# Optimization experiments

Hardware: AMD Instinct MI355X
Metric: run time of the kernel (lower is better)

The kernel has to match this reference:

```python
import jax, jax.numpy as jnp
import numpy as np
from jax import lax

RANK = 8
ALPHA = 16.0
SCALING = ALPHA / RANK  # 2.0
C_IN, C_OUT, KH, KW = 128, 256, 3, 3


def setup_inputs() -> dict:
    key = jax.random.key(0)
    k1, k2, k3, k4, k5 = jax.random.split(key, 5)
    x = jax.random.normal(k1, (16, C_IN, 64, 64), dtype=jnp.float32)
    W = jax.random.normal(k2, (C_OUT, C_IN, KH, KW), dtype=jnp.float32) * 0.05
    b = jax.random.normal(k3, (C_OUT,), dtype=jnp.float32) * 0.05
    lora_A = jax.random.normal(k4, (RANK, C_IN * KH * KW), dtype=jnp.float32) * 0.02
    lora_B = jax.random.normal(k5, (C_OUT, RANK), dtype=jnp.float32) * 0.02
    return {"x": x, "W": W, "b": b, "lora_A": lora_A, "lora_B": lora_B}


def _conv(x, w, stride=(1, 1), padding=((1, 1), (1, 1))):
    return lax.conv_general_dilated(
        x, w, window_strides=stride, padding=padding,
        dimension_numbers=("NCHW", "OIHW", "NCHW"))


def reference(x, W, b, lora_A, lora_B):
    # Base (frozen) conv: [B, C_out, H, W]
    base_out = _conv(x, W) + b[None, :, None, None]
    # LoRA path. The torch code does im2col -> (BL, C_in*kh*kw) @ A.T @ B.T.
    # Because unfold flattens patches channel-major as (C_in, kh, kw), the
    # identical math is: rank-r conv with A reshaped as [rank, C_in, kh, kw],
    # then a 1x1 mix with B. Same result, no im2col materialization.
    A_k = lora_A.reshape(RANK, C_IN, KH, KW)
    h = _conv(x, A_k)                                   # [B, rank, H, W]
    lora_out = jnp.einsum("brhw,or->bohw", h, lora_B) * SCALING
    return base_out + lora_out
```

## Files before the change

kernel.cpp:

```cpp
#include <hip/hip_runtime.h>
#include <hip/hip_bf16.h>


#define CIN   128
#define COUT  256
#define NBAT  16
#define HPAD  66
#define WPAD  66

typedef __bf16 bf16x8 __attribute__((ext_vector_type(8)));
typedef float f32x4 __attribute__((ext_vector_type(4)));

#define XPAD_ELEMS ((size_t)NBAT * HPAD * WPAD * CIN)
#define XPAD_BYTES (XPAD_ELEMS * 2)
#define WT_ELEMS   ((size_t)9 * COUT * CIN)
#define WS_NEED    (XPAD_BYTES + WT_ELEMS * 2)

typedef __attribute__((address_space(1))) void gvoid;
typedef __attribute__((address_space(3))) void lvoid;

__device__ __forceinline__ void load_lds16(const void* g, void* l) {
    __builtin_amdgcn_global_load_lds((gvoid*)g, (lvoid*)l, 16, 0, 0);
}

__global__ void prep_w(const float* __restrict__ W, const float* __restrict__ lA,
                       const float* __restrict__ lB, __hip_bfloat16* __restrict__ Wt) {
    int idx = blockIdx.x * 256 + threadIdx.x;
    int c   = idx & 127;
    int o   = (idx >> 7) & 255;
    int tap = idx >> 15;
    float acc = W[(o * 128 + c) * 9 + tap];
    float s = 0.f;
#pragma unroll
    for (int r = 0; r < 8; ++r)
        s += lB[o * 8 + r] * lA[r * 1152 + c * 9 + tap];
    acc += 2.0f * s;
    Wt[idx] = __float2bfloat16(acc);
}

__global__ void pad_x(const float* __restrict__ x, __bf16* __restrict__ xpad) {
    __shared__ float tile[128][66];
    const int n = blockIdx.x >> 6;
    const int h = blockIdx.x & 63;
    const int t = threadIdx.x;
    const float* src = x + (size_t)n * 128 * 4096 + (size_t)h * 64;
#pragma unroll
    for (int i = 0; i < 8; ++i) {
        int g  = i * 256 + t;
        int c  = g >> 4;
        int w4 = (g & 15) * 4;
        const float4 v = *reinterpret_cast<const float4*>(src + (size_t)c * 4096 + w4);
        tile[c][w4 + 0] = v.x; tile[c][w4 + 1] = v.y;
        tile[c][w4 + 2] = v.z; tile[c][w4 + 3] = v.w;
    }
    __syncthreads();
    __bf16* dst = xpad + ((size_t)(n * 66 + h + 1) * 66 + 1) * 128;
#pragma unroll
    for (int i = 0; i < 4; ++i) {
        int g  = i * 256 + t;
        int w  = g >> 4;
        int c0 = (g & 15) * 8;
        bf16x8 v;
#pragma unroll
        for (int j = 0; j < 8; ++j) v[j] = (__bf16)tile[c0 + j][w];
        *reinterpret_cast<bf16x8*>(dst + (size_t)w * 128 + c0) = v;
    }
    bf16x8 z = {};
    __bf16* rowbase = xpad + (size_t)(n * 66 + h + 1) * 66 * 128;
    if (t < 32) {
        int ww = (t < 16) ? 0 : 65;
        int c0 = (t & 15) * 8;
        *reinterpret_cast<bf16x8*>(rowbase + (size_t)ww * 128 + c0) = z;
    }
    if (h == 0 || h == 63) {
        __bf16* hrow = xpad + (size_t)(n * 66 + (h == 0 ? 0 : 65)) * 66 * 128;
        for (int i = t; i < 66 * 16; i += 256)
            *reinterpret_cast<bf16x8*>(hrow + (size_t)i * 8) = z;
    }
}

__global__ void __launch_bounds__(256) conv_mfma(
    const __bf16* __restrict__ xpad, const __bf16* __restrict__ Wt,
    const float* __restrict__ bias, float* __restrict__ out) {
    __shared__ __align__(16) __bf16 As[128 * 64];
    __shared__ __align__(16) __bf16 Bs[128 * 64];

    const int tid  = threadIdx.x;
    const int wv   = tid >> 6;
    const int lane = tid & 63;

    const int pt    = blockIdx.x;
    const int ob    = blockIdx.y;
    const int n     = pt >> 5;
    const int h0    = (pt & 31) << 1;
    const int obase = ob << 7;

    const int swz = ((lane >> 3) << 7) + ((((lane & 7) ^ (lane >> 3)) & 7) << 3);

    const __bf16* aG[4];
    const __bf16* bG[4];
#pragma unroll
    for (int j = 0; j < 4; ++j) {
        const int row0 = wv * 32 + j * 8;
        aG[j] = Wt + (obase + row0) * 128 + swz;
        const int p0 = row0;
        bG[j] = xpad + (((size_t)(n * 66 + h0 + (p0 >> 6)) * 66 + (p0 & 63)) * 128) + swz;
    }

    const int wo = (wv >> 1) << 6;
    const int wp = (wv & 1) << 6;

    int arow[4], brow[4], qo[2];
#pragma unroll
    for (int i = 0; i < 4; ++i) {
        arow[i] = (wo + i * 16 + (lane & 15)) << 6;
        brow[i] = (wp + i * 16 + (lane & 15)) << 6;
    }
#pragma unroll
    for (int s = 0; s < 2; ++s)
        qo[s] = ((((lane >> 4) + s * 4) ^ (lane & 7)) << 3);

    f32x4 acc[4][4] = {};

#pragma unroll
    for (int tap = 0; tap < 9; ++tap) {
        const int kh = tap / 3, kw = tap % 3;
        const int aoff_t = tap * (COUT * CIN);
        const int boff_t = (kh * 66 + kw) * 128;
#pragma unroll
        for (int cb = 0; cb < 2; ++cb) {
            const int ao = aoff_t + cb * 64;
            const int bo = boff_t + cb * 64;
            __syncthreads();
#pragma unroll
            for (int j = 0; j < 4; ++j) {
                load_lds16(aG[j] + ao, &As[wv * 2048 + j * 512]);
                load_lds16(bG[j] + bo, &Bs[wv * 2048 + j * 512]);
            }
            __syncthreads();
#pragma unroll
            for (int s = 0; s < 2; ++s) {
                bf16x8 af[4], bfr[4];
#pragma unroll
                for (int i = 0; i < 4; ++i) {
                    af[i]  = *reinterpret_cast<const bf16x8*>(&As[arow[i] + qo[s]]);
                    bfr[i] = *reinterpret_cast<const bf16x8*>(&Bs[brow[i] + qo[s]]);
                }
#pragma unroll
                for (int mi = 0; mi < 4; ++mi)
#pragma unroll
                    for (int ni = 0; ni < 4; ++ni)
                        acc[mi][ni] = __builtin_amdgcn_mfma_f32_16x16x32_bf16(
                            af[mi], bfr[ni], acc[mi][ni], 0, 0, 0);
            }
        }
    }

    const int col  = lane & 15;
    const int orow = (lane >> 4) << 2;
    const int h    = h0 + (wv & 1);
#pragma unroll
    for (int mi = 0; mi < 4; ++mi) {
        const int obm = obase + wo + mi * 16 + orow;
#pragma unroll
        for (int j = 0; j < 4; ++j) {
            const int o = obm + j;
            const float bj = bias[o];
            float* orow_ptr = out + (((size_t)n * 256 + o) * 64 + h) * 64;
#pragma unroll
            for (int ni = 0; ni < 4; ++ni)
                orow_ptr[ni * 16 + col] = acc[mi][ni][j] + bj;
        }
    }
}

__global__ void conv_naive(const float* __restrict__ x, const float* __restrict__ W,
                           const float* __restrict__ b, const float* __restrict__ lA,
                           const float* __restrict__ lB, float* __restrict__ out) {
    int idx = blockIdx.x * 256 + threadIdx.x;
    int w = idx & 63, h = (idx >> 6) & 63, o = (idx >> 12) & 255, n = idx >> 20;
    float acc = b[o];
    float hr[8] = {0, 0, 0, 0, 0, 0, 0, 0};
    for (int c = 0; c < 128; ++c)
        for (int kh = 0; kh < 3; ++kh) {
            int hy = h + kh - 1;
            if (hy < 0 || hy > 63) continue;
            for (int kw = 0; kw < 3; ++kw) {
                int wx = w + kw - 1;
                if (wx < 0 || wx > 63) continue;
                float xv = x[((n * 128 + c) * 64 + hy) * 64 + wx];
                int ka = c * 9 + kh * 3 + kw;
                acc += W[(o * 128 + c) * 9 + kh * 3 + kw] * xv;
#pragma unroll
                for (int r = 0; r < 8; ++r) hr[r] += lA[r * 1152 + ka] * xv;
            }
        }
    float ls = 0.f;
#pragma unroll
    for (int r = 0; r < 8; ++r) ls += lB[o * 8 + r] * hr[r];
    out[idx] = acc + 2.0f * ls;
}

extern "C" void kernel_launch(void* const* d_in, const int* in_sizes, int n_in,
                              void* d_out, int out_size, void* d_ws, size_t ws_size,
                              hipStream_t stream) {
    const float* x  = (const float*)d_in[0];
    const float* W  = (const float*)d_in[1];
    const float* b  = (const float*)d_in[2];
    const float* lA = (const float*)d_in[3];
    const float* lB = (const float*)d_in[4];
    float* out = (float*)d_out;

    if (ws_size < WS_NEED) {
        conv_naive<<<out_size / 256, 256, 0, stream>>>(x, W, b, lA, lB, out);
        return;
    }

    __bf16* xpad = (__bf16*)d_ws;
    __hip_bfloat16* Wt = (__hip_bfloat16*)((char*)d_ws + XPAD_BYTES);

    pad_x<<<NBAT * 64, 256, 0, stream>>>(x, xpad);
    prep_w<<<(int)(WT_ELEMS / 256), 256, 0, stream>>>(W, lA, lB, Wt);
    conv_mfma<<<dim3(512, 2), 256, 0, stream>>>(xpad, (const __bf16*)Wt, b, out);
}
```

Baseline: 144.4 us.

## Fuse pad, weight prep and conv into one cooperative kernel with grid sync

Merges the three launches (input pad/transposition to bf16, weight+LoRA folding, and the MFMA conv) into one cooperative kernel of 1024 blocks, with a grid-wide barrier between the prep phase and the conv phase. Shared memory is reused between the pad tile and the A/B conv tiles. The goal is to remove launch gaps and the tails between kernels. In exchange, all blocks must be co-resident (launch_bounds 256,4), the grid sync itself has a cost, and the conv phase loses scheduling freedom. If the cooperative launch fails, it falls back to the three separate kernels.

Result: slower. 371.7 us (+157.3%).

```diff
diff --git a/kernel.cpp b/kernel.cpp
--- a/kernel.cpp
+++ b/kernel.cpp
@@ -1,17 +1,16 @@
 #include <hip/hip_runtime.h>
 #include <hip/hip_bf16.h>
+#include <hip/hip_cooperative_groups.h>
 
 
 #define CIN   128
 #define COUT  256
 #define NBAT  16
-#define HPAD  66
-#define WPAD  66
 
 typedef __bf16 bf16x8 __attribute__((ext_vector_type(8)));
 typedef float f32x4 __attribute__((ext_vector_type(4)));
 
-#define XPAD_ELEMS ((size_t)NBAT * HPAD * WPAD * CIN)
+#define XPAD_ELEMS ((size_t)NBAT * 66 * 66 * CIN)
 #define XPAD_BYTES (XPAD_ELEMS * 2)
 #define WT_ELEMS   ((size_t)9 * COUT * CIN)
 #define WS_NEED    (XPAD_BYTES + WT_ELEMS * 2)
@@ -23,9 +22,11 @@
     __builtin_amdgcn_global_load_lds((gvoid*)g, (lvoid*)l, 16, 0, 0);
 }
 
-__global__ void prep_w(const float* __restrict__ W, const float* __restrict__ lA,
-                       const float* __restrict__ lB, __hip_bfloat16* __restrict__ Wt) {
-    int idx = blockIdx.x * 256 + threadIdx.x;
+
+__device__ __forceinline__ void prepw_body(const float* __restrict__ W,
+                                           const float* __restrict__ lA,
+                                           const float* __restrict__ lB,
+                                           __hip_bfloat16* __restrict__ Wt, int idx) {
     int c   = idx & 127;
     int o   = (idx >> 7) & 255;
     int tap = idx >> 15;
@@ -38,11 +39,9 @@
     Wt[idx] = __float2bfloat16(acc);
 }
 
-__global__ void pad_x(const float* __restrict__ x, __bf16* __restrict__ xpad) {
-    __shared__ float tile[128][66];
-    const int n = blockIdx.x >> 6;
-    const int h = blockIdx.x & 63;
-    const int t = threadIdx.x;
+__device__ __forceinline__ void pad_body(const float* __restrict__ x,
+                                         __bf16* __restrict__ xpad,
+                                         float (*tile)[66], int n, int h, int t) {
     const float* src = x + (size_t)n * 128 * 4096 + (size_t)h * 64;
 #pragma unroll
     for (int i = 0; i < 8; ++i) {
@@ -79,18 +78,14 @@
     }
 }
 
-__global__ void __launch_bounds__(256) conv_mfma(
-    const __bf16* __restrict__ xpad, const __bf16* __restrict__ Wt,
-    const float* __restrict__ bias, float* __restrict__ out) {
-    __shared__ __align__(16) __bf16 As[128 * 64];
-    __shared__ __align__(16) __bf16 Bs[128 * 64];
-
-    const int tid  = threadIdx.x;
+__device__ __forceinline__ void conv_body(const __bf16* __restrict__ xpad,
+                                          const __bf16* __restrict__ Wt,
+                                          const float* __restrict__ bias,
+                                          float* __restrict__ out,
+                                          __bf16* As, __bf16* Bs,
+                                          int pt, int ob, int tid) {
     const int wv   = tid >> 6;
     const int lane = tid & 63;
-
-    const int pt    = blockIdx.x;
-    const int ob    = blockIdx.y;
     const int n     = pt >> 5;
     const int h0    = (pt & 31) << 1;
     const int obase = ob << 7;
@@ -134,8 +129,8 @@
             __syncthreads();
 #pragma unroll
             for (int j = 0; j < 4; ++j) {
-                load_lds16(aG[j] + ao, &As[wv * 2048 + j * 512]);
-                load_lds16(bG[j] + bo, &Bs[wv * 2048 + j * 512]);
+                load_lds16(aG[j] + ao, As + wv * 2048 + j * 512);
+                load_lds16(bG[j] + bo, Bs + wv * 2048 + j * 512);
             }
             __syncthreads();
 #pragma unroll
@@ -143,8 +138,8 @@
                 bf16x8 af[4], bfr[4];
 #pragma unroll
                 for (int i = 0; i < 4; ++i) {
-                    af[i]  = *reinterpret_cast<const bf16x8*>(&As[arow[i] + qo[s]]);
-                    bfr[i] = *reinterpret_cast<const bf16x8*>(&Bs[brow[i] + qo[s]]);
+                    af[i]  = *reinterpret_cast<const bf16x8*>(As + arow[i] + qo[s]);
+                    bfr[i] = *reinterpret_cast<const bf16x8*>(Bs + brow[i] + qo[s]);
                 }
 #pragma unroll
                 for (int mi = 0; mi < 4; ++mi)
@@ -172,6 +167,43 @@
                 orow_ptr[ni * 16 + col] = acc[mi][ni][j] + bj;
         }
     }
+}
+
+__global__ void __launch_bounds__(256, 4) fused_kernel(
+    const float* __restrict__ x, const float* __restrict__ W,
+    const float* __restrict__ b, const float* __restrict__ lA,
+    const float* __restrict__ lB, __bf16* __restrict__ xpad,
+    __hip_bfloat16* __restrict__ Wt, float* __restrict__ out) {
+    __shared__ __align__(16) unsigned char smem[128 * 66 * 4];
+    const int bid = blockIdx.x;
+    const int t   = threadIdx.x;
+
+    pad_body(x, xpad, reinterpret_cast<float(*)[66]>(smem), bid >> 6, bid & 63, t);
+    for (int chunk = bid; chunk < 1152; chunk += 1024)
+        prepw_body(W, lA, lB, Wt, chunk * 256 + t);
+
+    __threadfence();
+    cooperative_groups::this_grid().sync();
+
+    conv_body(xpad, (const __bf16*)Wt, b, out,
+              (__bf16*)smem, (__bf16*)smem + 8192, bid & 511, bid >> 9, t);
+}
+
+__global__ void pad_x(const float* __restrict__ x, __bf16* __restrict__ xpad) {
+    __shared__ float tile[128][66];
+    pad_body(x, xpad, tile, blockIdx.x >> 6, blockIdx.x & 63, threadIdx.x);
+}
+
+__global__ void prep_w(const float* __restrict__ W, const float* __restrict__ lA,
+                       const float* __restrict__ lB, __hip_bfloat16* __restrict__ Wt) {
+    prepw_body(W, lA, lB, Wt, blockIdx.x * 256 + threadIdx.x);
+}
+
+__global__ void __launch_bounds__(256) conv_mfma(
+    const __bf16* __restrict__ xpad, const __bf16* __restrict__ Wt,
+    const float* __restrict__ bias, float* __restrict__ out) {
+    __shared__ __align__(16) __bf16 AB[2][8192];
+    conv_body(xpad, Wt, bias, out, AB[0], AB[1], blockIdx.x, blockIdx.y, threadIdx.x);
 }
 
 __global__ void conv_naive(const float* __restrict__ x, const float* __restrict__ W,
@@ -219,7 +251,13 @@
     __bf16* xpad = (__bf16*)d_ws;
     __hip_bfloat16* Wt = (__hip_bfloat16*)((char*)d_ws + XPAD_BYTES);
 
-    pad_x<<<NBAT * 64, 256, 0, stream>>>(x, xpad);
-    prep_w<<<(int)(WT_ELEMS / 256), 256, 0, stream>>>(W, lA, lB, Wt);
-    conv_mfma<<<dim3(512, 2), 256, 0, stream>>>(xpad, (const __bf16*)Wt, b, out);
-}
+    void* args[] = {(void*)&x, (void*)&W, (void*)&b, (void*)&lA, (void*)&lB,
+                    (void*)&xpad, (void*)&Wt, (void*)&out};
+    hipError_t err = hipLaunchCooperativeKernel(fused_kernel, dim3(1024), dim3(256),
+                                                args, 0, stream);
+    if (err != hipSuccess) {
+        pad_x<<<NBAT * 64, 256, 0, stream>>>(x, xpad);
+        prep_w<<<(int)(WT_ELEMS / 256), 256, 0, stream>>>(W, lA, lB, Wt);
+        conv_mfma<<<dim3(512, 2), 256, 0, stream>>>(xpad, (const __bf16*)Wt, b, out);
+    }
+}
```

## Fuse pad and weight prep; replace LDS-tiled conv with register-direct single-wave blocks

Applied to the files above, without the earlier changes.

Merges the input padding and weight-prep kernels into one launch, removing a kernel launch. The main conv kernel drops the LDS staging and barriers. Each single-wave block now loads MFMA operands straight from global memory into registers and computes a 64x64 output tile over 4096 blocks. This trades LDS reuse and large tiles for no synchronisation and more blocks, but it relies on L2/L1 to absorb the repeated global loads and may stall on load latency without explicit pipelining.

New measurement: 233.5 us. +61.6%, slower.

```diff
diff --git a/kernel.cpp b/kernel.cpp
--- a/kernel.cpp
+++ b/kernel.cpp
@@ -5,44 +5,24 @@
 #define CIN   128
 #define COUT  256
 #define NBAT  16
-#define HPAD  66
-#define WPAD  66
 
 typedef __bf16 bf16x8 __attribute__((ext_vector_type(8)));
 typedef float f32x4 __attribute__((ext_vector_type(4)));
 
-#define XPAD_ELEMS ((size_t)NBAT * HPAD * WPAD * CIN)
+#define XPAD_ELEMS ((size_t)NBAT * 66 * 66 * CIN)
 #define XPAD_BYTES (XPAD_ELEMS * 2)
 #define WT_ELEMS   ((size_t)9 * COUT * CIN)
 #define WS_NEED    (XPAD_BYTES + WT_ELEMS * 2)
 
-typedef __attribute__((address_space(1))) void gvoid;
-typedef __attribute__((address_space(3))) void lvoid;
+__global__ void pad_prep(const float* __restrict__ x, const float* __restrict__ W,
+                         const float* __restrict__ lA, const float* __restrict__ lB,
+                         __bf16* __restrict__ xpad, __bf16* __restrict__ Wt) {
+    __shared__ float tile[128][66];
+    const int bid = blockIdx.x;
+    const int n = bid >> 6;
+    const int h = bid & 63;
+    const int t = threadIdx.x;
 
-__device__ __forceinline__ void load_lds16(const void* g, void* l) {
-    __builtin_amdgcn_global_load_lds((gvoid*)g, (lvoid*)l, 16, 0, 0);
-}
-
-__global__ void prep_w(const float* __restrict__ W, const float* __restrict__ lA,
-                       const float* __restrict__ lB, __hip_bfloat16* __restrict__ Wt) {
-    int idx = blockIdx.x * 256 + threadIdx.x;
-    int c   = idx & 127;
-    int o   = (idx >> 7) & 255;
-    int tap = idx >> 15;
-    float acc = W[(o * 128 + c) * 9 + tap];
-    float s = 0.f;
-#pragma unroll
-    for (int r = 0; r < 8; ++r)
-        s += lB[o * 8 + r] * lA[r * 1152 + c * 9 + tap];
-    acc += 2.0f * s;
-    Wt[idx] = __float2bfloat16(acc);
-}
-
-__global__ void pad_x(const float* __restrict__ x, __bf16* __restrict__ xpad) {
-    __shared__ float tile[128][66];
-    const int n = blockIdx.x >> 6;
-    const int h = blockIdx.x & 63;
-    const int t = threadIdx.x;
     const float* src = x + (size_t)n * 128 * 4096 + (size_t)h * 64;
 #pragma unroll
     for (int i = 0; i < 8; ++i) {
@@ -77,99 +57,83 @@
         for (int i = t; i < 66 * 16; i += 256)
             *reinterpret_cast<bf16x8*>(hrow + (size_t)i * 8) = z;
     }
+
+    for (int chunk = bid; chunk < 1152; chunk += 1024) {
+        int idx = chunk * 256 + t;
+        int c   = idx & 127;
+        int o   = (idx >> 7) & 255;
+        int tap = idx >> 15;
+        float acc = W[(o * 128 + c) * 9 + tap];
+        float s = 0.f;
+#pragma unroll
+        for (int r = 0; r < 8; ++r)
+            s += lB[o * 8 + r] * lA[r * 1152 + c * 9 + tap];
+        Wt[idx] = (__bf16)(acc + 2.0f * s);
+    }
 }
 
-__global__ void __launch_bounds__(256) conv_mfma(
+__global__ void __launch_bounds__(64, 3) conv_rdirect(
     const __bf16* __restrict__ xpad, const __bf16* __restrict__ Wt,
     const float* __restrict__ bias, float* __restrict__ out) {
-    __shared__ __align__(16) __bf16 As[128 * 64];
-    __shared__ __align__(16) __bf16 Bs[128 * 64];
+    const int bid = blockIdx.x;
+    const int p   = bid & 7;
+    const int nb  = (bid >> 3) & 3;
+    const int r   = bid >> 5;
+    const int pt  = (r << 3) | p;
+    const int n   = pt >> 6;
+    const int h   = pt & 63;
+    const int obase = nb << 6;
 
-    const int tid  = threadIdx.x;
-    const int wv   = tid >> 6;
-    const int lane = tid & 63;
+    const int lane = threadIdx.x;
+    const int m    = lane & 15;
+    const int kq   = (lane >> 4) * 8;
 
-    const int pt    = blockIdx.x;
-    const int ob    = blockIdx.y;
-    const int n     = pt >> 5;
-    const int h0    = (pt & 31) << 1;
-    const int obase = ob << 7;
-
-    const int swz = ((lane >> 3) << 7) + ((((lane & 7) ^ (lane >> 3)) & 7) << 3);
-
-    const __bf16* aG[4];
-    const __bf16* bG[4];
-#pragma unroll
-    for (int j = 0; j < 4; ++j) {
-        const int row0 = wv * 32 + j * 8;
-        aG[j] = Wt + (obase + row0) * 128 + swz;
-        const int p0 = row0;
-        bG[j] = xpad + (((size_t)(n * 66 + h0 + (p0 >> 6)) * 66 + (p0 & 63)) * 128) + swz;
-    }
-
-    const int wo = (wv >> 1) << 6;
-    const int wp = (wv & 1) << 6;
-
-    int arow[4], brow[4], qo[2];
-#pragma unroll
-    for (int i = 0; i < 4; ++i) {
-        arow[i] = (wo + i * 16 + (lane & 15)) << 6;
-        brow[i] = (wp + i * 16 + (lane & 15)) << 6;
-    }
-#pragma unroll
-    for (int s = 0; s < 2; ++s)
-        qo[s] = ((((lane >> 4) + s * 4) ^ (lane & 7)) << 3);
+    const __bf16* aB = Wt + (obase + m) * 128 + kq;
+    const __bf16* bB = xpad + ((size_t)(n * 66 + h) * 66 + m) * 128 + kq;
 
     f32x4 acc[4][4] = {};
 
 #pragma unroll
-    for (int tap = 0; tap < 9; ++tap) {
-        const int kh = tap / 3, kw = tap % 3;
-        const int aoff_t = tap * (COUT * CIN);
-        const int boff_t = (kh * 66 + kw) * 128;
+    for (int kh = 0; kh < 3; ++kh) {
 #pragma unroll
-        for (int cb = 0; cb < 2; ++cb) {
-            const int ao = aoff_t + cb * 64;
-            const int bo = boff_t + cb * 64;
-            __syncthreads();
+        for (int kw = 0; kw < 3; ++kw) {
+            const int tap = kh * 3 + kw;
+            const __bf16* a0 = aB + tap * (COUT * CIN);
+            const __bf16* b0 = bB + (kh * 66 + kw) * 128;
 #pragma unroll
-            for (int j = 0; j < 4; ++j) {
-                load_lds16(aG[j] + ao, &As[wv * 2048 + j * 512]);
-                load_lds16(bG[j] + bo, &Bs[wv * 2048 + j * 512]);
-            }
-            __syncthreads();
+            for (int cb = 0; cb < 2; ++cb) {
+                bf16x8 af[4][2], bfr[4][2];
 #pragma unroll
-            for (int s = 0; s < 2; ++s) {
-                bf16x8 af[4], bfr[4];
+                for (int i = 0; i < 4; ++i)
 #pragma unroll
-                for (int i = 0; i < 4; ++i) {
-                    af[i]  = *reinterpret_cast<const bf16x8*>(&As[arow[i] + qo[s]]);
-                    bfr[i] = *reinterpret_cast<const bf16x8*>(&Bs[brow[i] + qo[s]]);
-                }
+                    for (int s = 0; s < 2; ++s) {
+                        af[i][s]  = *reinterpret_cast<const bf16x8*>(a0 + i * 2048 + cb * 64 + s * 32);
+                        bfr[i][s] = *reinterpret_cast<const bf16x8*>(b0 + i * 2048 + cb * 64 + s * 32);
+                    }
 #pragma unroll
-                for (int mi = 0; mi < 4; ++mi)
+                for (int s = 0; s < 2; ++s)
 #pragma unroll
-                    for (int ni = 0; ni < 4; ++ni)
-                        acc[mi][ni] = __builtin_amdgcn_mfma_f32_16x16x32_bf16(
-                            af[mi], bfr[ni], acc[mi][ni], 0, 0, 0);
+                    for (int mi = 0; mi < 4; ++mi)
+#pragma unroll
+                        for (int ni = 0; ni < 4; ++ni)
+                            acc[mi][ni] = __builtin_amdgcn_mfma_f32_16x16x32_bf16(
+                                af[mi][s], bfr[ni][s], acc[mi][ni], 0, 0, 0);
             }
         }
     }
 
-    const int col  = lane & 15;
     const int orow = (lane >> 4) << 2;
-    const int h    = h0 + (wv & 1);
 #pragma unroll
     for (int mi = 0; mi < 4; ++mi) {
-        const int obm = obase + wo + mi * 16 + orow;
+        const int obm = obase + mi * 16 + orow;
 #pragma unroll
         for (int j = 0; j < 4; ++j) {
             const int o = obm + j;
             const float bj = bias[o];
-            float* orow_ptr = out + (((size_t)n * 256 + o) * 64 + h) * 64;
+            float* op = out + (((size_t)n * 256 + o) * 64 + h) * 64;
 #pragma unroll
             for (int ni = 0; ni < 4; ++ni)
-                orow_ptr[ni * 16 + col] = acc[mi][ni][j] + bj;
+                op[ni * 16 + m] = acc[mi][ni][j] + bj;
         }
     }
 }
@@ -217,9 +181,8 @@
     }
 
     __bf16* xpad = (__bf16*)d_ws;
-    __hip_bfloat16* Wt = (__hip_bfloat16*)((char*)d_ws + XPAD_BYTES);
+    __bf16* Wt   = (__bf16*)((char*)d_ws + XPAD_BYTES);
 
-    pad_x<<<NBAT * 64, 256, 0, stream>>>(x, xpad);
-    prep_w<<<(int)(WT_ELEMS / 256), 256, 0, stream>>>(W, lA, lB, Wt);
-    conv_mfma<<<dim3(512, 2), 256, 0, stream>>>(xpad, (const __bf16*)Wt, b, out);
+    pad_prep<<<1024, 256, 0, stream>>>(x, W, lA, lB, xpad, Wt);
+    conv_rdirect<<<4096, 64, 0, stream>>>(xpad, Wt, b, out);
 }
```
